# Optimization experiments

Hardware: AMD Instinct MI355X
Metric: run time of the kernel (lower is better)

The kernel has to match this reference:

```python
import jax, jax.numpy as jnp
import numpy as np


def setup_inputs() -> dict:
    key = jax.random.key(0)
    k0, k1, k2, k3 = jax.random.split(key, 4)
    B, M, H, K, OUT = 256, 64, 64, 128, 256
    x0 = jax.random.normal(k0, (B, M, K), dtype=jnp.float32)
    xl = jax.random.normal(k1, (B, H, K), dtype=jnp.float32)
    # Conv1d(in_channels=M*H, out_channels=OUT, kernel_size=1) params
    fan_in = M * H  # kernel_size=1
    bound = 1.0 / np.sqrt(fan_in)
    W = jax.random.uniform(k2, (OUT, M * H, 1), dtype=jnp.float32, minval=-bound, maxval=bound)
    b = jax.random.uniform(k3, (OUT,), dtype=jnp.float32, minval=-bound, maxval=bound)
    return {"x0": x0, "xl": xl, "k": K, "W": W, "b": b}


def reference(x0, xl, k, W, b):
    # x0: [B, m, k_emb], xl: [B, h, k_emb]
    # Fused equivalent of the per-column loop: for each embedding column i,
    # matmul(xl[:,:,i:i+1], x0[:,:,i:i+1]^T) -> [B,h,m]; stacked over k -> [B,h,m,k]
    fmap = jnp.einsum('bhk,bmk->bhmk', xl, x0)
    B = x0.shape[0]
    h, m = xl.shape[1], x0.shape[1]
    fmap = fmap.reshape(B, h * m, k)  # [B, h*m, k]
    # 1x1 Conv1d == GEMM over channel dim
    out = jnp.einsum('bck,oc->bok', fmap, W[:, :, 0]) + b[None, :, None]
    return out
```

## Files before the change

### kernel.cpp

```cpp
#include <hip/hip_runtime.h>
#include <hip/hip_bf16.h>
#include <stdint.h>


typedef __attribute__((ext_vector_type(8)))  short short8;
typedef __attribute__((ext_vector_type(16))) float f32x16;

#define B_SZ   256
#define K_SZ   128
#define OUT_SZ 256
#define C_SZ   4096
#define NH     64

__device__ __forceinline__ uint32_t pack_bf16(float a, float b) {
    __hip_bfloat162 h2 = __float22bfloat162_rn(make_float2(a, b));
    union { __hip_bfloat162 h; uint32_t u; } v;
    v.h = h2;
    return v.u;
}

__device__ __forceinline__ float bf2f(short s) {
    union { uint32_t u; float f; } v;
    v.u = ((uint32_t)(uint16_t)s) << 16;
    return v.f;
}

__device__ __forceinline__ void load_lds_16(const void* g, void* l) {
    __builtin_amdgcn_global_load_lds(
        (const __attribute__((address_space(1))) unsigned int*)g,
        (__attribute__((address_space(3))) unsigned int*)l,
        16, 0, 0);
}

__global__ void convert_W_tiled(const float* __restrict__ W, short* __restrict__ Wb) {
    int t = blockIdx.x * blockDim.x + threadIdx.x;
    int lane = t & 63;
    int sub  = t >> 6;
    int cb16 = sub & 255;
    int got  = sub >> 8;
    int o = got * 32 + (lane & 31);
    int c = cb16 * 16 + (lane >> 5) * 8;
    const float* p = W + (size_t)o * C_SZ + c;
    float4 w0 = *(const float4*)p;
    float4 w1 = *(const float4*)(p + 4);
    union { short8 s; uint32_t u[4]; } cc;
    cc.u[0] = pack_bf16(w0.x, w0.y);
    cc.u[1] = pack_bf16(w0.z, w0.w);
    cc.u[2] = pack_bf16(w1.x, w1.y);
    cc.u[3] = pack_bf16(w1.z, w1.w);
    *(short8*)(Wb + (size_t)t * 8) = cc.s;
}

template<bool USE_WS>
__global__ __launch_bounds__(256, 2)
void cin_main(const float* __restrict__ x0, const float* __restrict__ xl,
              const float* __restrict__ Wf, const short* __restrict__ Wb,
              const float* __restrict__ bias, float* __restrict__ out) {
    __shared__ short Wlds[4 * 2 * 2048];
    __shared__ short xls[NH * K_SZ];

    const int b     = blockIdx.y;
    const int ohalf = blockIdx.x;
    const int tid   = threadIdx.x;
    const int lane  = tid & 63;
    const int wave  = tid >> 6;
    const int got   = ohalf * 4 + wave;
    const int l31   = lane & 31;
    const int hi    = lane >> 5;

    {
        const float4* src = (const float4*)(xl + (size_t)b * (NH * K_SZ));
        uint32_t* dst = (uint32_t*)&xls[tid * 32];
#pragma unroll
        for (int i = 0; i < 8; ++i) {
            float4 v = src[tid * 8 + i];
            dst[2 * i]     = pack_bf16(v.x, v.y);
            dst[2 * i + 1] = pack_bf16(v.z, v.w);
        }
    }

    union { short8 s; uint32_t u[4]; } x0p[4][4];
    {
        const float* x0b = x0 + (size_t)b * (64 * K_SZ);
#pragma unroll
        for (int s = 0; s < 4; ++s)
#pragma unroll
            for (int nt = 0; nt < 4; ++nt)
#pragma unroll
                for (int t2 = 0; t2 < 4; ++t2) {
                    const int m0 = s * 16 + hi * 8 + 2 * t2;
                    const int cc = nt * 32 + l31;
                    x0p[s][nt].u[t2] = pack_bf16(x0b[m0 * K_SZ + cc],
                                                 x0b[(m0 + 1) * K_SZ + cc]);
                }
    }

    const short* wsrc  = Wb + ((size_t)got * 256) * 512 + lane * 8;
    const float* wfrow = Wf + (size_t)(got * 32 + l31) * C_SZ + hi * 8;
    short* wl = Wlds + wave * (2 * 2048);

    auto stage = [&](int buf, int h) {
        if (USE_WS) {
            const short* s0 = wsrc + (size_t)(4 * h) * 512;
            short* d = wl + buf * 2048;
#pragma unroll
            for (int sub = 0; sub < 4; ++sub)
                load_lds_16(s0 + sub * 512, d + sub * 512);
        } else {
#pragma unroll
            for (int sub = 0; sub < 4; ++sub) {
                const float* p = wfrow + h * 64 + sub * 16;
                float4 w0 = *(const float4*)p;
                float4 w1 = *(const float4*)(p + 4);
                union { short8 s; uint32_t u[4]; } cc;
                cc.u[0] = pack_bf16(w0.x, w0.y);
                cc.u[1] = pack_bf16(w0.z, w0.w);
                cc.u[2] = pack_bf16(w1.x, w1.y);
                cc.u[3] = pack_bf16(w1.z, w1.w);
                *(short8*)(wl + buf * 2048 + sub * 512 + lane * 8) = cc.s;
            }
        }
    };

    f32x16 acc[4];
#pragma unroll
    for (int nt = 0; nt < 4; ++nt)
#pragma unroll
        for (int r = 0; r < 16; ++r) acc[nt][r] = 0.f;
    f32x16 kz;
#pragma unroll
    for (int r = 0; r < 16; ++r) kz[r] = 0.f;

    stage(0, 0);
    stage(1, 1);
    __syncthreads();

    f32x16 gE = kz, gO = kz;
    float px2 = 0.f, px3 = 0.f;

#define CHAIN(G, NT)                                                                   \
    do {                                                                               \
        G = __builtin_amdgcn_mfma_f32_32x32x16_bf16(af0, x0p[0][NT].s, kz, 0, 0, 0);   \
        G = __builtin_amdgcn_mfma_f32_32x32x16_bf16(af1, x0p[1][NT].s, G, 0, 0, 0);    \
        G = __builtin_amdgcn_mfma_f32_32x32x16_bf16(af2, x0p[2][NT].s, G, 0, 0, 0);    \
        G = __builtin_amdgcn_mfma_f32_32x32x16_bf16(af3, x0p[3][NT].s, G, 0, 0, 0);    \
    } while (0)

#define TAIL(ACC_I, PX, G)                                                             \
    do {                                                                               \
        _Pragma("unroll")                                                              \
        for (int r = 0; r < 16; ++r) acc[ACC_I][r] += (PX) * G[r];                     \
    } while (0)

    for (int h = 0; h < NH; ++h) {
        if (USE_WS) asm volatile("s_waitcnt vmcnt(4)" ::: "memory");

        const short* wb2 = wl + (h & 1) * 2048 + lane * 8;
        const short8 af0 = *(const short8*)(wb2);
        const short8 af1 = *(const short8*)(wb2 + 512);
        const short8 af2 = *(const short8*)(wb2 + 1024);
        const short8 af3 = *(const short8*)(wb2 + 1536);

        const float xlv0 = bf2f(xls[h * K_SZ + 0 * 32 + l31]);
        const float xlv1 = bf2f(xls[h * K_SZ + 1 * 32 + l31]);
        const float xlv2 = bf2f(xls[h * K_SZ + 2 * 32 + l31]);
        const float xlv3 = bf2f(xls[h * K_SZ + 3 * 32 + l31]);

        __builtin_amdgcn_s_setprio(1);
        TAIL(2, px2, gE);
        CHAIN(gE, 0);
        TAIL(3, px3, gO);
        CHAIN(gO, 1);
        TAIL(0, xlv0, gE);
        CHAIN(gE, 2);
        TAIL(1, xlv1, gO);
        CHAIN(gO, 3);
        __builtin_amdgcn_s_setprio(0);

        px2 = xlv2;
        px3 = xlv3;

        asm volatile("s_waitcnt lgkmcnt(0)" ::: "memory");
        stage(h & 1, (h + 2) & (NH - 1));
    }

    TAIL(2, px2, gE);
    TAIL(3, px3, gO);
#undef CHAIN
#undef TAIL

    float bv[16];
#pragma unroll
    for (int r = 0; r < 16; ++r)
        bv[r] = bias[got * 32 + (r & 3) + 8 * (r >> 2) + 4 * hi];

    float* outb = out + (size_t)b * (OUT_SZ * K_SZ);
#pragma unroll
    for (int nt = 0; nt < 4; ++nt) {
        const int kcol = nt * 32 + l31;
#pragma unroll
        for (int r = 0; r < 16; ++r) {
            const int orow = got * 32 + (r & 3) + 8 * (r >> 2) + 4 * hi;
            outb[orow * K_SZ + kcol] = acc[nt][r] + bv[r];
        }
    }
}

extern "C" void kernel_launch(void* const* d_in, const int* in_sizes, int n_in,
                              void* d_out, int out_size, void* d_ws, size_t ws_size,
                              hipStream_t stream) {
    const float* x0   = (const float*)d_in[0];
    const float* xl   = (const float*)d_in[1];
    const float* W    = (const float*)d_in[3];
    const float* bias = (const float*)d_in[4];
    float* out = (float*)d_out;

    const size_t w_bytes = (size_t)OUT_SZ * C_SZ * sizeof(short);
    short* Wb = (short*)d_ws;

    if (ws_size >= w_bytes) {
        convert_W_tiled<<<dim3(512), dim3(256), 0, stream>>>(W, Wb);
        cin_main<true><<<dim3(2, B_SZ), dim3(256), 0, stream>>>(x0, xl, W, Wb, bias, out);
    } else {
        cin_main<false><<<dim3(2, B_SZ), dim3(256), 0, stream>>>(x0, xl, W, Wb, bias, out);
    }
}
```

Before: 81.71 us.

## Split k dimension across blocks to double grid and cut per-thread registers

Each block now handles half of the k columns (64 instead of 128), so the grid doubles to 4x256 blocks and per-thread accumulators and x0 fragments halve. Launch bounds are raised to 3 blocks per CU to exploit the lower register and LDS footprint. The cost is that the W tiles are streamed from L2 twice as often per batch, and each h iteration now has only two MFMA chains, leaving less work to hide the LDS staging latency.

```diff
diff --git a/kernel.cpp b/kernel.cpp
--- a/kernel.cpp
+++ b/kernel.cpp
@@ -52,15 +52,18 @@
 }
 
 template<bool USE_WS>
-__global__ __launch_bounds__(256, 2)
+__global__ __launch_bounds__(256, 3)
 void cin_main(const float* __restrict__ x0, const float* __restrict__ xl,
               const float* __restrict__ Wf, const short* __restrict__ Wb,
               const float* __restrict__ bias, float* __restrict__ out) {
     __shared__ short Wlds[4 * 2 * 2048];
-    __shared__ short xls[NH * K_SZ];
+    __shared__ short xls[NH * 64];
 
     const int b     = blockIdx.y;
-    const int ohalf = blockIdx.x;
+    const int bx    = blockIdx.x;
+    const int ohalf = bx >> 1;
+    const int khalf = bx & 1;
+    const int kb    = khalf * 64;
     const int tid   = threadIdx.x;
     const int lane  = tid & 63;
     const int wave  = tid >> 6;
@@ -69,27 +72,30 @@
     const int hi    = lane >> 5;
 
     {
-        const float4* src = (const float4*)(xl + (size_t)b * (NH * K_SZ));
-        uint32_t* dst = (uint32_t*)&xls[tid * 32];
-#pragma unroll
-        for (int i = 0; i < 8; ++i) {
-            float4 v = src[tid * 8 + i];
+        const float* xlb = xl + (size_t)b * (NH * K_SZ);
+        const int h    = tid >> 2;
+        const int koff = (tid & 3) * 16;
+        const float4* src = (const float4*)(xlb + h * K_SZ + kb + koff);
+        uint32_t* dst = (uint32_t*)&xls[h * 64 + koff];
+#pragma unroll
+        for (int i = 0; i < 4; ++i) {
+            float4 v = src[i];
             dst[2 * i]     = pack_bf16(v.x, v.y);
             dst[2 * i + 1] = pack_bf16(v.z, v.w);
         }
     }
 
-    union { short8 s; uint32_t u[4]; } x0p[4][4];
+    union { short8 s; uint32_t u[4]; } x0p[4][2];
     {
         const float* x0b = x0 + (size_t)b * (64 * K_SZ);
 #pragma unroll
         for (int s = 0; s < 4; ++s)
 #pragma unroll
-            for (int nt = 0; nt < 4; ++nt)
+            for (int nt = 0; nt < 2; ++nt)
 #pragma unroll
                 for (int t2 = 0; t2 < 4; ++t2) {
                     const int m0 = s * 16 + hi * 8 + 2 * t2;
-                    const int cc = nt * 32 + l31;
+                    const int cc = kb + nt * 32 + l31;
                     x0p[s][nt].u[t2] = pack_bf16(x0b[m0 * K_SZ + cc],
                                                  x0b[(m0 + 1) * K_SZ + cc]);
                 }
@@ -122,9 +128,9 @@
         }
     };
 
-    f32x16 acc[4];
-#pragma unroll
-    for (int nt = 0; nt < 4; ++nt)
+    f32x16 acc[2];
+#pragma unroll
+    for (int nt = 0; nt < 2; ++nt)
 #pragma unroll
         for (int r = 0; r < 16; ++r) acc[nt][r] = 0.f;
     f32x16 kz;
@@ -136,7 +142,7 @@
     __syncthreads();
 
     f32x16 gE = kz, gO = kz;
-    float px2 = 0.f, px3 = 0.f;
+    float px0 = 0.f, px1 = 0.f;
 
 #define CHAIN(G, NT)                                                                   \
     do {                                                                               \
@@ -161,31 +167,25 @@
         const short8 af2 = *(const short8*)(wb2 + 1024);
         const short8 af3 = *(const short8*)(wb2 + 1536);
 
-        const float xlv0 = bf2f(xls[h * K_SZ + 0 * 32 + l31]);
-        const float xlv1 = bf2f(xls[h * K_SZ + 1 * 32 + l31]);
-        const float xlv2 = bf2f(xls[h * K_SZ + 2 * 32 + l31]);
-        const float xlv3 = bf2f(xls[h * K_SZ + 3 * 32 + l31]);
+        const float xlv0 = bf2f(xls[h * 64 + 0 * 32 + l31]);
+        const float xlv1 = bf2f(xls[h * 64 + 1 * 32 + l31]);
 
         __builtin_amdgcn_s_setprio(1);
-        TAIL(2, px2, gE);
+        TAIL(0, px0, gE);
         CHAIN(gE, 0);
-        TAIL(3, px3, gO);
+        TAIL(1, px1, gO);
         CHAIN(gO, 1);
-        TAIL(0, xlv0, gE);
-        CHAIN(gE, 2);
-        TAIL(1, xlv1, gO);
-        CHAIN(gO, 3);
         __builtin_amdgcn_s_setprio(0);
 
-        px2 = xlv2;
-        px3 = xlv3;
+        px0 = xlv0;
+        px1 = xlv1;
 
         asm volatile("s_waitcnt lgkmcnt(0)" ::: "memory");
         stage(h & 1, (h + 2) & (NH - 1));
     }
 
-    TAIL(2, px2, gE);
-    TAIL(3, px3, gO);
+    TAIL(0, px0, gE);
+    TAIL(1, px1, gO);
 #undef CHAIN
 #undef TAIL
 
@@ -196,8 +196,8 @@
 
     float* outb = out + (size_t)b * (OUT_SZ * K_SZ);
 #pragma unroll
-    for (int nt = 0; nt < 4; ++nt) {
-        const int kcol = nt * 32 + l31;
+    for (int nt = 0; nt < 2; ++nt) {
+        const int kcol = kb + nt * 32 + l31;
 #pragma unroll
         for (int r = 0; r < 16; ++r) {
             const int orow = got * 32 + (r & 3) + 8 * (r >> 2) + 4 * hi;
@@ -220,8 +220,8 @@
 
     if (ws_size >= w_bytes) {
         convert_W_tiled<<<dim3(512), dim3(256), 0, stream>>>(W, Wb);
-        cin_main<true><<<dim3(2, B_SZ), dim3(256), 0, stream>>>(x0, xl, W, Wb, bias, out);
+        cin_main<true><<<dim3(4, B_SZ), dim3(256), 0, stream>>>(x0, xl, W, Wb, bias, out);
     } else {
-        cin_main<false><<<dim3(2, B_SZ), dim3(256), 0, stream>>>(x0, xl, W, Wb, bias, out);
-    }
-}
+        cin_main<false><<<dim3(4, B_SZ), dim3(256), 0, stream>>>(x0, xl, W, Wb, bias, out);
+    }
+}
```

Measured after the change: 88.54 us. 8.4% more time.
